# Performance work log

Hardware: AMD Instinct MI355X
Metric: run time of the kernel (lower is better)

The kernel has to match this reference:

```python
import jax, jax.numpy as jnp
import numpy as np

N_HEAD = 16
LORA_SCALE = 1.0 / 4.0  # alpha=1, r=4
LN_EPS = 1e-5


def _ln(x, g, b):
    # LayerNorm subclass casts to float32 then back to input dtype
    xf = x.astype(jnp.float32)
    m = xf.mean(-1, keepdims=True)
    v = xf.var(-1, keepdims=True)
    y = (xf - m) / jnp.sqrt(v + LN_EPS) * g + b
    return y.astype(x.dtype)


def _lora(h, a, b):
    # x @ a.T @ b.T * scaling ; a:[r,d], b:[d,r]
    return (h @ a.T) @ b.T * LORA_SCALE


def _attn(h, Wq, bq, Wk, Wv, bv, Wo, bo, la_k, lb_k, la_v, lb_v, la_o, lb_o):
    B, S, D = h.shape
    hd = D // N_HEAD
    scale = hd ** (-0.25)
    q = h @ Wq.T + bq
    k = h @ Wk.T + _lora(h, la_k, lb_k)          # key Linear has no bias
    v = h @ Wv.T + bv + _lora(h, la_v, lb_v)
    qh = q.reshape(B, S, N_HEAD, hd).transpose(0, 2, 1, 3) * scale  # [B,H,S,hd]
    kh = k.reshape(B, S, N_HEAD, hd).transpose(0, 2, 1, 3) * scale
    vh = v.reshape(B, S, N_HEAD, hd).transpose(0, 2, 1, 3)
    qk = jnp.einsum('bhqd,bhkd->bhqk', qh, kh).astype(jnp.float32)
    w = jax.nn.softmax(qk, axis=-1).astype(q.dtype)
    wv = jnp.einsum('bhqk,bhkd->bhqd', w, vh)
    wv = wv.transpose(0, 2, 1, 3).reshape(B, S, D)
    return wv @ Wo.T + bo + _lora(wv, la_o, lb_o)


def setup_inputs() -> dict:
    key = jax.random.key(0)
    D, R = 1024, 4
    B, S = 8, 1024
    ks = jax.random.split(key, 20)
    sd = 0.02
    inp = {
        'x': jax.random.normal(ks[0], (B, S, D), jnp.float32),
        'Wq': jax.random.normal(ks[1], (D, D), jnp.float32) * sd,
        'bq': jnp.zeros((D,), jnp.float32),
        'Wk': jax.random.normal(ks[2], (D, D), jnp.float32) * sd,
        'Wv': jax.random.normal(ks[3], (D, D), jnp.float32) * sd,
        'bv': jnp.zeros((D,), jnp.float32),
        'Wo': jax.random.normal(ks[4], (D, D), jnp.float32) * sd,
        'bo': jnp.zeros((D,), jnp.float32),
        'la_k': jax.random.normal(ks[5], (R, D), jnp.float32) * sd,
        'lb_k': jax.random.normal(ks[6], (D, R), jnp.float32) * sd,
        'la_v': jax.random.normal(ks[7], (R, D), jnp.float32) * sd,
        'lb_v': jax.random.normal(ks[8], (D, R), jnp.float32) * sd,
        'la_o': jax.random.normal(ks[9], (R, D), jnp.float32) * sd,
        'lb_o': jax.random.normal(ks[10], (D, R), jnp.float32) * sd,
        'g_attn': jnp.ones((D,), jnp.float32),
        'b_attn': jnp.zeros((D,), jnp.float32),
        'W1': jax.random.normal(ks[11], (4 * D, D), jnp.float32) * sd,
        'b1': jnp.zeros((4 * D,), jnp.float32),
        'W2': jax.random.normal(ks[12], (D, 4 * D), jnp.float32) * sd,
        'b2': jnp.zeros((D,), jnp.float32),
        'g_mlp': jnp.ones((D,), jnp.float32),
        'b_mlp': jnp.zeros((D,), jnp.float32),
    }
    return inp


def reference(x, Wq, bq, Wk, Wv, bv, Wo, bo, la_k, lb_k, la_v, lb_v, la_o, lb_o,
              g_attn, b_attn, W1, b1, W2, b2, g_mlp, b_mlp):
    # self-attention + residual (LoRA on key/value/out)
    x = x + _attn(_ln(x, g_attn, b_attn), Wq, bq, Wk, Wv, bv, Wo, bo,
                  la_k, lb_k, la_v, lb_v, la_o, lb_o)
    # MLP + residual (exact GELU, matching nn.GELU default)
    h = _ln(x, g_mlp, b_mlp)
    h = jax.nn.gelu(h @ W1.T + b1, approximate=False)
    x = x + h @ W2.T + b2
    return x
```

## Files before the change

kernel.cpp:

```cpp
#include <hip/hip_runtime.h>
#include <math.h>

typedef _Float16 f16_t;
typedef f16_t f16x8 __attribute__((ext_vector_type(8)));
typedef f16_t f16x4 __attribute__((ext_vector_type(4)));
typedef float f32x4 __attribute__((ext_vector_type(4)));
typedef float fv4 __attribute__((ext_vector_type(4)));

#define MFMA16(a, b, c) __builtin_amdgcn_mfma_f32_16x16x32_f16(a, b, c, 0, 0, 0)

__device__ __forceinline__ void gload16(const void* g, void* l) {
  __builtin_amdgcn_global_load_lds((const __attribute__((address_space(1))) void*)g,
                                   (__attribute__((address_space(3))) void*)l, 16, 0, 0);
}

__global__ __launch_bounds__(256) void ln_f32(const float* __restrict__ x,
                                              const float* __restrict__ g,
                                              const float* __restrict__ b,
                                              f16_t* __restrict__ y) {
  const int D = 1024;
  int row = blockIdx.x;
  int t = threadIdx.x;
  const float* xr = x + (size_t)row * D + t * 4;
  float x0 = xr[0], x1 = xr[1], x2 = xr[2], x3 = xr[3];
  float sum = x0 + x1 + x2 + x3;
  float sq = x0 * x0 + x1 * x1 + x2 * x2 + x3 * x3;
  for (int d = 32; d; d >>= 1) {
    sum += __shfl_down(sum, d);
    sq += __shfl_down(sq, d);
  }
  __shared__ float ssum[4], ssq[4];
  int w = t >> 6, lane = t & 63;
  if (lane == 0) { ssum[w] = sum; ssq[w] = sq; }
  __syncthreads();
  float ts = ssum[0] + ssum[1] + ssum[2] + ssum[3];
  float tq = ssq[0] + ssq[1] + ssq[2] + ssq[3];
  float mean = ts * (1.0f / 1024.0f);
  float var = tq * (1.0f / 1024.0f) - mean * mean;
  float rstd = rsqrtf(var + 1e-5f);
  f16_t* yr = y + (size_t)row * D + t * 4;
  const float* gr = g + t * 4;
  const float* br = b + t * 4;
  yr[0] = (f16_t)((x0 - mean) * rstd * gr[0] + br[0]);
  yr[1] = (f16_t)((x1 - mean) * rstd * gr[1] + br[1]);
  yr[2] = (f16_t)((x2 - mean) * rstd * gr[2] + br[2]);
  yr[3] = (f16_t)((x3 - mean) * rstd * gr[3] + br[3]);
}

__global__ __launch_bounds__(256) void ln_f16(const f16_t* __restrict__ x,
                                              const float* __restrict__ g,
                                              const float* __restrict__ b,
                                              f16_t* __restrict__ y) {
  const int D = 1024;
  int row = blockIdx.x;
  int t = threadIdx.x;
  const f16_t* xr = x + (size_t)row * D + t * 4;
  float x0 = (float)xr[0], x1 = (float)xr[1], x2 = (float)xr[2], x3 = (float)xr[3];
  float sum = x0 + x1 + x2 + x3;
  float sq = x0 * x0 + x1 * x1 + x2 * x2 + x3 * x3;
  for (int d = 32; d; d >>= 1) {
    sum += __shfl_down(sum, d);
    sq += __shfl_down(sq, d);
  }
  __shared__ float ssum[4], ssq[4];
  int w = t >> 6, lane = t & 63;
  if (lane == 0) { ssum[w] = sum; ssq[w] = sq; }
  __syncthreads();
  float ts = ssum[0] + ssum[1] + ssum[2] + ssum[3];
  float tq = ssq[0] + ssq[1] + ssq[2] + ssq[3];
  float mean = ts * (1.0f / 1024.0f);
  float var = tq * (1.0f / 1024.0f) - mean * mean;
  float rstd = rsqrtf(var + 1e-5f);
  f16_t* yr = y + (size_t)row * D + t * 4;
  const float* gr = g + t * 4;
  const float* br = b + t * 4;
  yr[0] = (f16_t)((x0 - mean) * rstd * gr[0] + br[0]);
  yr[1] = (f16_t)((x1 - mean) * rstd * gr[1] + br[1]);
  yr[2] = (f16_t)((x2 - mean) * rstd * gr[2] + br[2]);
  yr[3] = (f16_t)((x3 - mean) * rstd * gr[3] + br[3]);
}

__global__ __launch_bounds__(256) void convert_w(
    const float* __restrict__ wq, const float* __restrict__ wk,
    const float* __restrict__ wv, const float* __restrict__ wo,
    const float* __restrict__ w1, const float* __restrict__ w2,
    f16_t* __restrict__ oq, f16_t* __restrict__ ok, f16_t* __restrict__ ov,
    f16_t* __restrict__ oo, f16_t* __restrict__ o1, f16_t* __restrict__ o2) {
  int bid = blockIdx.x;
  const float* src;
  f16_t* dst;
  int bi;
  if (bid < 2048) {
    int seg = bid >> 9;
    bi = bid & 511;
    src = seg == 0 ? wq : seg == 1 ? wk : seg == 2 ? wv : wo;
    dst = seg == 0 ? oq : seg == 1 ? ok : seg == 2 ? ov : oo;
  } else if (bid < 4096) {
    bi = bid - 2048; src = w1; dst = o1;
  } else {
    bi = bid - 4096; src = w2; dst = o2;
  }
  size_t idx = (size_t)bi * 2048 + (size_t)threadIdx.x * 8;
  fv4 a = *(const fv4*)(src + idx);
  fv4 b = *(const fv4*)(src + idx + 4);
  f16x8 h;
#pragma unroll
  for (int j = 0; j < 4; ++j) { h[j] = (f16_t)a[j]; h[4 + j] = (f16_t)b[j]; }
  *(f16x8*)(dst + idx) = h;
}

__global__ __launch_bounds__(256) void lora_kv_kernel(
    const f16_t* __restrict__ h, const float* __restrict__ la_k,
    const float* __restrict__ la_v, float* __restrict__ t_k,
    float* __restrict__ t_v, int K) {
  int lane = threadIdx.x & 63;
  int w = threadIdx.x >> 6;
  int row = blockIdx.x * 4 + w;
  const f16_t* hrow = h + (size_t)row * K;
  float ak[4] = {0.f, 0.f, 0.f, 0.f};
  float av[4] = {0.f, 0.f, 0.f, 0.f};
  for (int it = 0; it < K / 512; ++it) {
    int base = it * 512 + lane * 8;
    f16x8 hx = *(const f16x8*)(hrow + base);
#pragma unroll
    for (int r = 0; r < 4; ++r) {
      const float* kr = la_k + (size_t)r * K + base;
      const float* vr = la_v + (size_t)r * K + base;
#pragma unroll
      for (int j = 0; j < 8; ++j) {
        float hv = (float)hx[j];
        ak[r] += hv * kr[j];
        av[r] += hv * vr[j];
      }
    }
  }
#pragma unroll
  for (int r = 0; r < 4; ++r) {
    for (int d = 32; d; d >>= 1) {
      ak[r] += __shfl_down(ak[r], d);
      av[r] += __shfl_down(av[r], d);
    }
  }
  if (lane == 0) {
#pragma unroll
    for (int r = 0; r < 4; ++r) {
      t_k[(size_t)row * 4 + r] = ak[r];
      t_v[(size_t)row * 4 + r] = av[r];
    }
  }
}

__global__ __launch_bounds__(256) void lora_t_kernel(const f16_t* __restrict__ h,
                                                     const float* __restrict__ la,
                                                     float* __restrict__ t, int K) {
  int lane = threadIdx.x & 63;
  int w = threadIdx.x >> 6;
  int row = blockIdx.x * 4 + w;
  const f16_t* hrow = h + (size_t)row * K;
  float acc[4] = {0.f, 0.f, 0.f, 0.f};
  for (int it = 0; it < K / 512; ++it) {
    int base = it * 512 + lane * 8;
    f16x8 hx = *(const f16x8*)(hrow + base);
#pragma unroll
    for (int r = 0; r < 4; ++r) {
      const float* ar = la + (size_t)r * K + base;
#pragma unroll
      for (int j = 0; j < 8; ++j) acc[r] += (float)hx[j] * ar[j];
    }
  }
#pragma unroll
  for (int r = 0; r < 4; ++r) {
    for (int d = 32; d; d >>= 1) acc[r] += __shfl_down(acc[r], d);
  }
  if (lane == 0) {
#pragma unroll
    for (int r = 0; r < 4; ++r) t[(size_t)row * 4 + r] = acc[r];
  }
}

__global__ __launch_bounds__(512, 2) void gemm_wide(
    const f16_t* __restrict__ A, const f16_t* __restrict__ B,
    const float* __restrict__ bias, const float* __restrict__ loraT,
    const float* __restrict__ loraB, const float* residf,
    const f16_t* __restrict__ residb, f16_t* Cb, float* Cf,
    int M, int N, int K, int ldb, int dogelu) {
  __shared__ __align__(16) f16_t Asm[8192];
  __shared__ __align__(16) f16_t Bsm[16384];
  const int tid = threadIdx.x;
  const int lane = tid & 63, wid = tid >> 6;
  const int wm = wid >> 2, wn = wid & 3;
  const int l15 = lane & 15, lhi = lane >> 4;
  int nwg = gridDim.x * gridDim.y;
  int bid = blockIdx.y * gridDim.x + blockIdx.x;
  int swz = (bid & 7) * (nwg >> 3) + (bid >> 3);
  const int m0 = (swz / gridDim.x) * 128, n0 = (swz % gridDim.x) * 256;
  const int arow = tid >> 3;
  const int aslot = tid & 7;

  f32x4 acc[4][4];
#pragma unroll
  for (int i = 0; i < 4; ++i)
#pragma unroll
    for (int j = 0; j < 4; ++j) acc[i][j] = (f32x4){0.f, 0.f, 0.f, 0.f};

  auto stageA = [&](int step) {
#pragma unroll
    for (int c = 0; c < 2; ++c) {
      int r = c * 64 + arow;
      int cm = aslot ^ (r & 7);
      gload16(A + (size_t)(m0 + r) * K + (size_t)step * 64 + cm * 8,
              (char*)Asm + c * 8192 + wid * 1024);
    }
  };
  auto stageB = [&](int step) {
#pragma unroll
    for (int c = 0; c < 4; ++c) {
      int r = c * 64 + arow;
      int cm = aslot ^ (r & 7);
      gload16(B + (size_t)(n0 + r) * ldb + (size_t)step * 64 + cm * 8,
              (char*)Bsm + c * 8192 + wid * 1024);
    }
  };

  const int nsteps = K >> 6;
  for (int t = 0; t < nsteps; ++t) {
    if (t) __syncthreads();
    stageA(t);
    stageB(t);
    __syncthreads();
#pragma unroll
    for (int kk = 0; kk < 2; ++kk) {
      f16x8 af[4], bf[4];
#pragma unroll
      for (int i = 0; i < 4; ++i) {
        int row = wm * 64 + i * 16 + l15;
        af[i] = *(const f16x8*)((char*)Asm + row * 128 +
                                ((kk * 64 + lhi * 16) ^ ((row & 7) << 4)));
      }
#pragma unroll
      for (int j = 0; j < 4; ++j) {
        int row = wn * 64 + j * 16 + l15;
        bf[j] = *(const f16x8*)((char*)Bsm + row * 128 +
                                ((kk * 64 + lhi * 16) ^ ((row & 7) << 4)));
      }
#pragma unroll
      for (int i = 0; i < 4; ++i)
#pragma unroll
        for (int j = 0; j < 4; ++j) acc[i][j] = MFMA16(af[i], bf[j], acc[i][j]);
    }
  }

  const int gm = m0 + wm * 64, gn = n0 + wn * 64;
#pragma unroll
  for (int j = 0; j < 4; ++j) {
    int gcol = gn + j * 16 + l15;
    float bj = bias ? bias[gcol] : 0.f;
    float lb0 = 0.f, lb1 = 0.f, lb2 = 0.f, lb3 = 0.f;
    if (loraB) {
      const float* p = loraB + (size_t)gcol * 4;
      lb0 = p[0]; lb1 = p[1]; lb2 = p[2]; lb3 = p[3];
    }
#pragma unroll
    for (int i = 0; i < 4; ++i) {
      float v4[4];
#pragma unroll
      for (int r = 0; r < 4; ++r) {
        int grow = gm + i * 16 + lhi * 4 + r;
        float val = acc[i][j][r] + bj;
        if (loraT) {
          const float* tp = loraT + (size_t)grow * 4;
          val += 0.25f * (tp[0] * lb0 + tp[1] * lb1 + tp[2] * lb2 + tp[3] * lb3);
        }
        if (dogelu) val = 0.5f * val * (1.0f + erff(val * 0.70710678118654752f));
        if (residf) val += residf[(size_t)grow * N + gcol];
        if (residb) val += (float)residb[(size_t)grow * N + gcol];
        v4[r] = val;
      }
      if (Cf) {
#pragma unroll
        for (int r = 0; r < 4; ++r)
          Cf[(size_t)(gm + i * 16 + lhi * 4 + r) * N + gcol] = v4[r];
      } else {
#pragma unroll
        for (int r = 0; r < 4; ++r)
          Cb[(size_t)(gm + i * 16 + lhi * 4 + r) * N + gcol] = (f16_t)v4[r];
      }
    }
  }
}

__global__ __launch_bounds__(512, 2) void gemm_qkv_wide(
    const f16_t* __restrict__ A, const f16_t* __restrict__ W,
    const float* __restrict__ bq, const float* __restrict__ bv,
    const float* __restrict__ t_k, const float* __restrict__ lb_k,
    const float* __restrict__ t_v, const float* __restrict__ lb_v,
    f16_t* __restrict__ Pq, f16_t* __restrict__ Pk, f16_t* __restrict__ Pvt,
    int K) {
  const int D = 1024;
  __shared__ __align__(16) f16_t Asm[8192];
  __shared__ __align__(16) f16_t Bsm[16384];
  const int tid = threadIdx.x;
  const int lane = tid & 63, wid = tid >> 6;
  const int wm = wid >> 2, wn = wid & 3;
  const int l15 = lane & 15, lhi = lane >> 4;
  int nwg = gridDim.x * gridDim.y;
  int bid = blockIdx.y * gridDim.x + blockIdx.x;
  int swz = (bid & 7) * (nwg >> 3) + (bid >> 3);
  const int m0 = (swz / gridDim.x) * 128, n0 = (swz % gridDim.x) * 256;
  const int seg = n0 >> 10;
  const int arow = tid >> 3;
  const int aslot = tid & 7;

  f32x4 acc[4][4];
#pragma unroll
  for (int i = 0; i < 4; ++i)
#pragma unroll
    for (int j = 0; j < 4; ++j) acc[i][j] = (f32x4){0.f, 0.f, 0.f, 0.f};

  auto stageA = [&](int step) {
#pragma unroll
    for (int c = 0; c < 2; ++c) {
      int r = c * 64 + arow;
      int cm = aslot ^ (r & 7);
      gload16(A + (size_t)(m0 + r) * K + (size_t)step * 64 + cm * 8,
              (char*)Asm + c * 8192 + wid * 1024);
    }
  };
  auto stageB = [&](int step) {
#pragma unroll
    for (int c = 0; c < 4; ++c) {
      int r = c * 64 + arow;
      int cm = aslot ^ (r & 7);
      gload16(W + (size_t)(n0 + r) * K + (size_t)step * 64 + cm * 8,
              (char*)Bsm + c * 8192 + wid * 1024);
    }
  };

  const int nsteps = K >> 6;
  for (int t = 0; t < nsteps; ++t) {
    if (t) __syncthreads();
    stageA(t);
    stageB(t);
    __syncthreads();
#pragma unroll
    for (int kk = 0; kk < 2; ++kk) {
      f16x8 af[4], bf[4];
#pragma unroll
      for (int i = 0; i < 4; ++i) {
        int row = wm * 64 + i * 16 + l15;
        af[i] = *(const f16x8*)((char*)Asm + row * 128 +
                                ((kk * 64 + lhi * 16) ^ ((row & 7) << 4)));
      }
#pragma unroll
      for (int j = 0; j < 4; ++j) {
        int row = wn * 64 + j * 16 + l15;
        bf[j] = *(const f16x8*)((char*)Bsm + row * 128 +
                                ((kk * 64 + lhi * 16) ^ ((row & 7) << 4)));
      }
#pragma unroll
      for (int i = 0; i < 4; ++i)
#pragma unroll
        for (int j = 0; j < 4; ++j) acc[i][j] = MFMA16(af[i], bf[j], acc[i][j]);
    }
  }

  const int gm = m0 + wm * 64, gn = n0 + wn * 64;
  const float* tB = (seg == 1) ? t_k : t_v;
#pragma unroll
  for (int j = 0; j < 4; ++j) {
    int gcol = gn + j * 16 + l15;
    int c = gcol & 1023;
    float bj = (seg == 0) ? bq[c] : (seg == 2 ? bv[c] : 0.f);
    float lb0 = 0.f, lb1 = 0.f, lb2 = 0.f, lb3 = 0.f;
    if (seg) {
      const float* p = (seg == 1 ? lb_k : lb_v) + (size_t)c * 4;
      lb0 = p[0]; lb1 = p[1]; lb2 = p[2]; lb3 = p[3];
    }
#pragma unroll
    for (int i = 0; i < 4; ++i) {
      float v4[4];
#pragma unroll
      for (int r = 0; r < 4; ++r) {
        int grow = gm + i * 16 + lhi * 4 + r;
        float val = acc[i][j][r] + bj;
        if (seg) {
          const float* tp = tB + (size_t)grow * 4;
          val += 0.25f * (tp[0] * lb0 + tp[1] * lb1 + tp[2] * lb2 + tp[3] * lb3);
        }
        v4[r] = val;
      }
      if (seg < 2) {
        f16_t* dst = (seg == 0) ? Pq : Pk;
#pragma unroll
        for (int r = 0; r < 4; ++r)
          dst[(size_t)(gm + i * 16 + lhi * 4 + r) * D + c] = (f16_t)v4[r];
      } else {
        int grow0 = gm + i * 16 + lhi * 4;
        int bb = grow0 >> 10, ss = grow0 & 1023;
        int hh = c >> 6, dd = c & 63;
        f16x4 pk;
#pragma unroll
        for (int r = 0; r < 4; ++r) pk[r] = (f16_t)v4[r];
        *(f16x4*)(Pvt + (((size_t)bb * 16 + hh) * 64 + dd) * 1024 + ss) = pk;
      }
    }
  }
}

__global__ __launch_bounds__(256, 2) void gemm_mfma(
    const f16_t* __restrict__ A, const float* __restrict__ B,
    const float* __restrict__ bias, const float* __restrict__ loraT,
    const float* __restrict__ loraB, const float* residf,
    const f16_t* __restrict__ residb, f16_t* Cb, float* Cf, f16_t* Cvt,
    int M, int N, int K, int ldb, int dogelu) {
  __shared__ __align__(16) f16_t smem[2][16384];
  const int tid = threadIdx.x;
  const int lane = tid & 63, wid = tid >> 6;
  const int wm = wid >> 1, wn = wid & 1;
  const int l15 = lane & 15, lhi = lane >> 4;
  const int m0 = blockIdx.y * 128, n0 = blockIdx.x * 128;
  const int arow = tid >> 3;
  const int aslot = tid & 7;

  f32x4 acc[4][4];
#pragma unroll
  for (int i = 0; i < 4; ++i)
#pragma unroll
    for (int j = 0; j < 4; ++j) acc[i][j] = (f32x4){0.f, 0.f, 0.f, 0.f};

  fv4 breg[4][2];

  auto stageA = [&](int step, int buf) {
#pragma unroll
    for (int c = 0; c < 4; ++c) {
      int r = c * 32 + arow;
      int cm = aslot ^ (r & 7);
      gload16(A + (size_t)(m0 + r) * K + (size_t)step * 64 + cm * 8,
              (char*)&smem[buf][0] + c * 4096 + wid * 1024);
    }
  };
  auto loadB = [&](int step) {
#pragma unroll
    for (int c = 0; c < 4; ++c) {
      int r = c * 32 + arow;
      const float* gp = B + (size_t)(n0 + r) * ldb + (size_t)step * 64 + aslot * 8;
      breg[c][0] = *(const fv4*)gp;
      breg[c][1] = *(const fv4*)(gp + 4);
    }
  };
  auto writeB = [&](int buf) {
#pragma unroll
    for (int c = 0; c < 4; ++c) {
      int r = c * 32 + arow;
      f16x8 hh;
#pragma unroll
      for (int j = 0; j < 4; ++j) hh[j] = (f16_t)breg[c][0][j];
#pragma unroll
      for (int j = 0; j < 4; ++j) hh[4 + j] = (f16_t)breg[c][1][j];
      int boff = r * 128 + ((aslot * 16) ^ ((r & 7) << 4));
      *(f16x8*)((char*)&smem[buf][8192] + boff) = hh;
    }
  };

  const int nsteps = K >> 6;
  stageA(0, 0);
  loadB(0);
  writeB(0);
  __syncthreads();
  for (int t = 0; t < nsteps; ++t) {
    int cur = t & 1, nxt = cur ^ 1;
    if (t + 1 < nsteps) { stageA(t + 1, nxt); loadB(t + 1); }
    const char* As = (const char*)&smem[cur][0];
    const char* Bs = (const char*)&smem[cur][8192];
#pragma unroll
    for (int kk = 0; kk < 2; ++kk) {
      f16x8 af[4], bf[4];
#pragma unroll
      for (int i = 0; i < 4; ++i) {
        int row = wm * 64 + i * 16 + l15;
        af[i] = *(const f16x8*)(As + row * 128 + ((kk * 64 + lhi * 16) ^ ((row & 7) << 4)));
      }
#pragma unroll
      for (int j = 0; j < 4; ++j) {
        int row = wn * 64 + j * 16 + l15;
        bf[j] = *(const f16x8*)(Bs + row * 128 + ((kk * 64 + lhi * 16) ^ ((row & 7) << 4)));
      }
#pragma unroll
      for (int i = 0; i < 4; ++i)
#pragma unroll
        for (int j = 0; j < 4; ++j) acc[i][j] = MFMA16(af[i], bf[j], acc[i][j]);
    }
    if (t + 1 < nsteps) writeB(nxt);
    __syncthreads();
  }

  const int gm = m0 + wm * 64, gn = n0 + wn * 64;
#pragma unroll
  for (int j = 0; j < 4; ++j) {
    int gcol = gn + j * 16 + l15;
    float bj = bias ? bias[gcol] : 0.f;
    float lb0 = 0.f, lb1 = 0.f, lb2 = 0.f, lb3 = 0.f;
    if (loraB) {
      const float* p = loraB + (size_t)gcol * 4;
      lb0 = p[0]; lb1 = p[1]; lb2 = p[2]; lb3 = p[3];
    }
#pragma unroll
    for (int i = 0; i < 4; ++i) {
      float v4[4];
#pragma unroll
      for (int r = 0; r < 4; ++r) {
        int grow = gm + i * 16 + lhi * 4 + r;
        float val = acc[i][j][r] + bj;
        if (loraT) {
          const float* tp = loraT + (size_t)grow * 4;
          val += 0.25f * (tp[0] * lb0 + tp[1] * lb1 + tp[2] * lb2 + tp[3] * lb3);
        }
        if (dogelu) val = 0.5f * val * (1.0f + erff(val * 0.70710678118654752f));
        if (residf) val += residf[(size_t)grow * N + gcol];
        if (residb) val += (float)residb[(size_t)grow * N + gcol];
        v4[r] = val;
      }
      if (Cf) {
#pragma unroll
        for (int r = 0; r < 4; ++r)
          Cf[(size_t)(gm + i * 16 + lhi * 4 + r) * N + gcol] = v4[r];
      } else if (Cvt) {
        int grow0 = gm + i * 16 + lhi * 4;
        int bb = grow0 >> 10, ss = grow0 & 1023;
        int hh = gcol >> 6, dd = gcol & 63;
        f16x4 pk;
#pragma unroll
        for (int r = 0; r < 4; ++r) pk[r] = (f16_t)v4[r];
        *(f16x4*)(Cvt + (((size_t)bb * 16 + hh) * 64 + dd) * 1024 + ss) = pk;
      } else {
#pragma unroll
        for (int r = 0; r < 4; ++r)
          Cb[(size_t)(gm + i * 16 + lhi * 4 + r) * N + gcol] = (f16_t)v4[r];
      }
    }
  }
}

__global__ __launch_bounds__(256, 3) void attn_mfma(const f16_t* __restrict__ q,
                                                    const f16_t* __restrict__ k,
                                                    const f16_t* __restrict__ vt,
                                                    f16_t* __restrict__ wv) {
  const int S = 1024, D = 1024;
  __shared__ __align__(16) f16_t Qs[128 * 64];
  __shared__ __align__(16) f16_t SP[128 * 64];
  __shared__ __align__(16) f16_t Ks[64 * 64];
  __shared__ __align__(16) f16_t Vts[64 * 64];
  __shared__ float rsb[128];
  __shared__ float lib[128];
  const int tid = threadIdx.x, lane = tid & 63, w = tid >> 6;
  const int l15 = lane & 15, lhi = lane >> 4;
  const int q0 = blockIdx.x * 128;
  const int h = blockIdx.y, b = blockIdx.z;
  const f16_t* qg = q + ((size_t)b * S + q0) * D + h * 64;
  const f16_t* kg = k + (size_t)b * S * D + h * 64;
  const f16_t* vg = vt + ((size_t)b * 16 + h) * 64 * (size_t)S;

#pragma unroll
  for (int c = 0; c < 4; ++c) {
    int r = c * 32 + (tid >> 3), kc = tid & 7;
    f16x8 xx = *(const f16x8*)(qg + (size_t)r * D + kc * 8);
    *(f16x8*)((char*)Qs + r * 128 + ((kc * 16) ^ ((r & 7) << 4))) = xx;
  }
  __syncthreads();
  f16x8 qf[2][2];
#pragma unroll
  for (int i = 0; i < 2; ++i) {
    int row = w * 32 + i * 16 + l15;
#pragma unroll
    for (int kk = 0; kk < 2; ++kk)
      qf[i][kk] = *(const f16x8*)((char*)Qs + row * 128 +
                                  ((kk * 64 + lhi * 16) ^ ((row & 7) << 4)));
  }

  f32x4 oacc[2][4];
#pragma unroll
  for (int i = 0; i < 2; ++i)
#pragma unroll
    for (int j = 0; j < 4; ++j) oacc[i][j] = (f32x4){0.f, 0.f, 0.f, 0.f};
  float m_run = -1e30f, l_run = 0.f;
  const int myrow = w * 32 + (lane >> 1);
  const int half = lane & 1;

  for (int kv = 0; kv < 16; ++kv) {
    __syncthreads();
#pragma unroll
    for (int c = 0; c < 2; ++c) {
      int r = c * 32 + (tid >> 3), kc = tid & 7;
      f16x8 xk = *(const f16x8*)(kg + (size_t)(kv * 64 + r) * D + kc * 8);
      *(f16x8*)((char*)Ks + r * 128 + ((kc * 16) ^ ((r & 7) << 4))) = xk;
      f16x8 xv = *(const f16x8*)(vg + (size_t)r * S + kv * 64 + kc * 8);
      *(f16x8*)((char*)Vts + r * 128 + ((kc * 16) ^ ((r & 7) << 4))) = xv;
    }
    __syncthreads();
    f32x4 sacc[2][4];
#pragma unroll
    for (int i = 0; i < 2; ++i)
#pragma unroll
      for (int j = 0; j < 4; ++j) sacc[i][j] = (f32x4){0.f, 0.f, 0.f, 0.f};
#pragma unroll
    for (int kk = 0; kk < 2; ++kk) {
      f16x8 kf[4];
#pragma unroll
      for (int j = 0; j < 4; ++j) {
        int row = j * 16 + l15;
        kf[j] = *(const f16x8*)((char*)Ks + row * 128 +
                                ((kk * 64 + lhi * 16) ^ ((row & 7) << 4)));
      }
#pragma unroll
      for (int i = 0; i < 2; ++i)
#pragma unroll
        for (int j = 0; j < 4; ++j) sacc[i][j] = MFMA16(qf[i][kk], kf[j], sacc[i][j]);
    }
#pragma unroll
    for (int i = 0; i < 2; ++i)
#pragma unroll
      for (int j = 0; j < 4; ++j)
#pragma unroll
        for (int r = 0; r < 4; ++r) {
          int srow = w * 32 + i * 16 + lhi * 4 + r;
          int scol = j * 16 + l15;
          *(f16_t*)((char*)SP + srow * 128 + ((scol * 2) ^ ((srow & 7) << 4))) =
              (f16_t)(sacc[i][j][r] * 0.125f);
        }
    __syncthreads();
    f16x8 ch[4];
#pragma unroll
    for (int c = 0; c < 4; ++c)
      ch[c] = *(const f16x8*)((char*)SP + myrow * 128 +
                              ((half * 64 + c * 16) ^ ((myrow & 7) << 4)));
    float mt = -1e30f;
#pragma unroll
    for (int c = 0; c < 4; ++c)
#pragma unroll
      for (int e = 0; e < 8; ++e) mt = fmaxf(mt, (float)ch[c][e]);
    mt = fmaxf(mt, __shfl_xor(mt, 1));
    float mnew = fmaxf(m_run, mt);
    float resc = __expf(m_run - mnew);
    float lsum = 0.f;
#pragma unroll
    for (int c = 0; c < 4; ++c) {
      f16x8 p8;
#pragma unroll
      for (int e = 0; e < 8; ++e) {
        float p = __expf((float)ch[c][e] - mnew);
        lsum += p;
        p8[e] = (f16_t)p;
      }
      *(f16x8*)((char*)SP + myrow * 128 + ((half * 64 + c * 16) ^ ((myrow & 7) << 4))) = p8;
    }
    lsum += __shfl_xor(lsum, 1);
    l_run = l_run * resc + lsum;
    m_run = mnew;
    if (half == 0) rsb[myrow] = resc;
    __syncthreads();
#pragma unroll
    for (int i = 0; i < 2; ++i) {
      float f0 = rsb[w * 32 + i * 16 + lhi * 4 + 0];
      float f1 = rsb[w * 32 + i * 16 + lhi * 4 + 1];
      float f2 = rsb[w * 32 + i * 16 + lhi * 4 + 2];
      float f3 = rsb[w * 32 + i * 16 + lhi * 4 + 3];
#pragma unroll
      for (int j = 0; j < 4; ++j) {
        oacc[i][j][0] *= f0;
        oacc[i][j][1] *= f1;
        oacc[i][j][2] *= f2;
        oacc[i][j][3] *= f3;
      }
    }
#pragma unroll
    for (int kk = 0; kk < 2; ++kk) {
      f16x8 pa[2], vb[4];
#pragma unroll
      for (int i = 0; i < 2; ++i) {
        int row = w * 32 + i * 16 + l15;
        pa[i] = *(const f16x8*)((char*)SP + row * 128 +
                                ((kk * 64 + lhi * 16) ^ ((row & 7) << 4)));
      }
#pragma unroll
      for (int j = 0; j < 4; ++j) {
        int row = j * 16 + l15;
        vb[j] = *(const f16x8*)((char*)Vts + row * 128 +
                                ((kk * 64 + lhi * 16) ^ ((row & 7) << 4)));
      }
#pragma unroll
      for (int i = 0; i < 2; ++i)
#pragma unroll
        for (int j = 0; j < 4; ++j) oacc[i][j] = MFMA16(pa[i], vb[j], oacc[i][j]);
    }
  }
  if (half == 0) lib[myrow] = 1.f / l_run;
  __syncthreads();
#pragma unroll
  for (int i = 0; i < 2; ++i)
#pragma unroll
    for (int r = 0; r < 4; ++r) {
      int row = w * 32 + i * 16 + lhi * 4 + r;
      float li = lib[row];
      size_t base = ((size_t)b * S + q0 + row) * D + h * 64;
#pragma unroll
      for (int j = 0; j < 4; ++j)
        wv[base + j * 16 + l15] = (f16_t)(oacc[i][j][r] * li);
    }
}

extern "C" void kernel_launch(void* const* d_in, const int* in_sizes, int n_in,
                              void* d_out, int out_size, void* d_ws, size_t ws_size,
                              hipStream_t stream) {
  const int B = 8, S = 1024, D = 1024, F = 4096;
  const int M = B * S;

  const float* x = (const float*)d_in[0];
  const float* Wq = (const float*)d_in[1];
  const float* bq = (const float*)d_in[2];
  const float* Wk = (const float*)d_in[3];
  const float* Wv = (const float*)d_in[4];
  const float* bv = (const float*)d_in[5];
  const float* Wo = (const float*)d_in[6];
  const float* bo = (const float*)d_in[7];
  const float* la_k = (const float*)d_in[8];
  const float* lb_k = (const float*)d_in[9];
  const float* la_v = (const float*)d_in[10];
  const float* lb_v = (const float*)d_in[11];
  const float* la_o = (const float*)d_in[12];
  const float* lb_o = (const float*)d_in[13];
  const float* g_attn = (const float*)d_in[14];
  const float* b_attn = (const float*)d_in[15];
  const float* W1 = (const float*)d_in[16];
  const float* b1 = (const float*)d_in[17];
  const float* W2 = (const float*)d_in[18];
  const float* b2 = (const float*)d_in[19];
  const float* g_mlp = (const float*)d_in[20];
  const float* b_mlp = (const float*)d_in[21];

  float* t_k = (float*)((char*)d_ws + 16);
  float* t_v = t_k + (size_t)M * 4;
  float* t_o = t_v + (size_t)M * 4;
  const size_t MD = (size_t)M * D;
  f16_t* P0 = (f16_t*)((char*)d_ws + 409600);
  f16_t* P1 = P0 + MD;
  f16_t* P2 = P0 + 2 * MD;
  f16_t* P3 = P0 + 3 * MD;
  f16_t* Wqkvf = P0 + 4 * MD;
  f16_t* Wof = Wqkvf + 3 * (size_t)D * D;
  f16_t* W1f = Wof + (size_t)D * D;
  f16_t* W2f = W1f + (size_t)F * D;
  float* outf = (float*)d_out;
  const size_t need = 409600 + 4 * MD * sizeof(f16_t) +
                      (4 * (size_t)D * D + 2 * (size_t)F * D) * sizeof(f16_t);
  const bool f16w = ws_size >= need;

  if (f16w)
    convert_w<<<6144, 256, 0, stream>>>(
        Wq, Wk, Wv, Wo, W1, W2, Wqkvf, Wqkvf + (size_t)D * D,
        Wqkvf + 2 * (size_t)D * D, Wof, W1f, W2f);

  ln_f32<<<M, 256, 0, stream>>>(x, g_attn, b_attn, P0);
  lora_kv_kernel<<<M / 4, 256, 0, stream>>>(P0, la_k, la_v, t_k, t_v, D);
  if (f16w) {
    gemm_qkv_wide<<<dim3(12, 64), 512, 0, stream>>>(
        P0, Wqkvf, bq, bv, t_k, lb_k, t_v, lb_v, P1, P2, P3, D);
  } else {
    gemm_mfma<<<dim3(8, 64), 256, 0, stream>>>(
        P0, Wq, bq, nullptr, nullptr, nullptr, nullptr, P1, nullptr, nullptr,
        M, D, D, D, 0);
    gemm_mfma<<<dim3(8, 64), 256, 0, stream>>>(
        P0, Wk, nullptr, t_k, lb_k, nullptr, nullptr, P2, nullptr, nullptr,
        M, D, D, D, 0);
    gemm_mfma<<<dim3(8, 64), 256, 0, stream>>>(
        P0, Wv, bv, t_v, lb_v, nullptr, nullptr, nullptr, nullptr, P3,
        M, D, D, D, 0);
  }
  attn_mfma<<<dim3(8, 16, 8), 256, 0, stream>>>(P1, P2, P3, P0);
  lora_t_kernel<<<M / 4, 256, 0, stream>>>(P0, la_o, t_o, D);
  if (f16w)
    gemm_wide<<<dim3(4, 64), 512, 0, stream>>>(
        P0, Wof, bo, t_o, lb_o, x, nullptr, P3, nullptr, M, D, D, D, 0);
  else
    gemm_mfma<<<dim3(8, 64), 256, 0, stream>>>(
        P0, Wo, bo, t_o, lb_o, x, nullptr, P3, nullptr, nullptr, M, D, D, D, 0);
  ln_f16<<<M, 256, 0, stream>>>(P3, g_mlp, b_mlp, P0);
  if (f16w) {
    gemm_wide<<<dim3(8, 64), 512, 0, stream>>>(
        P0, W1f, b1, nullptr, nullptr, nullptr, nullptr, P1, nullptr,
        M, 2048, D, D, 1);
    gemm_wide<<<dim3(4, 64), 512, 0, stream>>>(
        P1, W2f, b2, nullptr, nullptr, nullptr, P3, nullptr, outf,
        M, D, 2048, F, 0);
    gemm_wide<<<dim3(8, 64), 512, 0, stream>>>(
        P0, W1f + (size_t)2048 * D, b1 + 2048, nullptr, nullptr, nullptr, nullptr,
        P1, nullptr, M, 2048, D, D, 1);
    gemm_wide<<<dim3(4, 64), 512, 0, stream>>>(
        P1, W2f + 2048, nullptr, nullptr, nullptr, outf, nullptr, nullptr, outf,
        M, D, 2048, F, 0);
  } else {
    gemm_mfma<<<dim3(16, 64), 256, 0, stream>>>(
        P0, W1, b1, nullptr, nullptr, nullptr, nullptr, P1, nullptr, nullptr,
        M, 2048, D, D, 1);
    gemm_mfma<<<dim3(8, 64), 256, 0, stream>>>(
        P1, W2, b2, nullptr, nullptr, nullptr, P3, nullptr, outf, nullptr,
        M, D, 2048, F, 0);
    gemm_mfma<<<dim3(16, 64), 256, 0, stream>>>(
        P0, W1 + (size_t)2048 * D, b1 + 2048, nullptr, nullptr, nullptr, nullptr,
        P1, nullptr, nullptr, M, 2048, D, D, 1);
    gemm_mfma<<<dim3(8, 64), 256, 0, stream>>>(
        P1, W2 + 2048, nullptr, nullptr, nullptr, outf, nullptr, nullptr, outf,
        nullptr, M, D, 2048, F, 0);
  }
}
```

Baseline: 706.1 us.

## Triple-buffer GEMM LDS tiles with async prefetch and explicit vmcnt waits

Replaces the load-then-compute GEMM main loop with a three-stage LDS ring that prefetches tiles up to three steps ahead. It uses explicit s_waitcnt vmcnt counts, raw barriers and MFMA priority boosting. The aim is to hide global-to-LDS latency behind MFMA work, which the previous single-buffered loop fully exposed. The cost is LDS use rising to about 144KB per block, which likely allows only one 512-thread block per CU despite the launch bound of two.

```diff
diff --git a/kernel.cpp b/kernel.cpp
--- a/kernel.cpp
+++ b/kernel.cpp
@@ -178,14 +178,60 @@
   }
 }
 
-__global__ __launch_bounds__(512, 2) void gemm_wide(
+#define GEMM_PIPE_BODY                                                        \
+  f32x4 acc[4][4];                                                            \
+  _Pragma("unroll") for (int i = 0; i < 4; ++i)                               \
+      _Pragma("unroll") for (int j = 0; j < 4; ++j)                           \
+          acc[i][j] = (f32x4){0.f, 0.f, 0.f, 0.f};                            \
+  const int nsteps = K >> 6;                                                  \
+  stageA(0, 0); stageB(0, 0);                                                 \
+  stageA(1, 1); stageB(1, 1);                                                 \
+  stageA(2, 2); stageB(2, 2);                                                 \
+  int b3 = 0;                                                                 \
+  for (int kt = 0; kt < nsteps; ++kt) {                                       \
+    if (kt + 2 < nsteps)                                                      \
+      asm volatile("s_waitcnt vmcnt(12)" ::: "memory");                       \
+    else if (kt + 1 < nsteps)                                                 \
+      asm volatile("s_waitcnt vmcnt(6)" ::: "memory");                        \
+    else                                                                      \
+      asm volatile("s_waitcnt vmcnt(0)" ::: "memory");                        \
+    __builtin_amdgcn_sched_barrier(0);                                        \
+    __builtin_amdgcn_s_barrier();                                             \
+    f16x8 af[4][2], bf[4][2];                                                 \
+    _Pragma("unroll") for (int kk = 0; kk < 2; ++kk) {                        \
+      _Pragma("unroll") for (int i = 0; i < 4; ++i) {                         \
+        int row = wm * 64 + i * 16 + l15;                                     \
+        af[i][kk] = *(const f16x8*)((const char*)Abuf[b3] + row * 128 +       \
+                                    ((kk * 64 + lhi * 16) ^ ((row & 7) << 4)));\
+      }                                                                       \
+      _Pragma("unroll") for (int j = 0; j < 4; ++j) {                         \
+        int row = wn * 64 + j * 16 + l15;                                     \
+        bf[j][kk] = *(const f16x8*)((const char*)Bbuf[b3] + row * 128 +       \
+                                    ((kk * 64 + lhi * 16) ^ ((row & 7) << 4)));\
+      }                                                                       \
+    }                                                                         \
+    asm volatile("s_waitcnt lgkmcnt(0)" ::: "memory");                        \
+    __builtin_amdgcn_sched_barrier(0);                                        \
+    __builtin_amdgcn_s_barrier();                                             \
+    if (kt + 3 < nsteps) { stageA(kt + 3, b3); stageB(kt + 3, b3); }          \
+    __builtin_amdgcn_sched_barrier(0);                                        \
+    __builtin_amdgcn_s_setprio(1);                                            \
+    _Pragma("unroll") for (int kk = 0; kk < 2; ++kk)                          \
+        _Pragma("unroll") for (int i = 0; i < 4; ++i)                         \
+            _Pragma("unroll") for (int j = 0; j < 4; ++j)                     \
+                acc[i][j] = MFMA16(af[i][kk], bf[j][kk], acc[i][j]);          \
+    __builtin_amdgcn_s_setprio(0);                                            \
+    b3 = (b3 == 2) ? 0 : b3 + 1;                                              \
+  }
+
+__global__ __launch_bounds__(512, 2) void gemm_pipe(
     const f16_t* __restrict__ A, const f16_t* __restrict__ B,
     const float* __restrict__ bias, const float* __restrict__ loraT,
     const float* __restrict__ loraB, const float* residf,
     const f16_t* __restrict__ residb, f16_t* Cb, float* Cf,
     int M, int N, int K, int ldb, int dogelu) {
-  __shared__ __align__(16) f16_t Asm[8192];
-  __shared__ __align__(16) f16_t Bsm[16384];
+  __shared__ __align__(16) f16_t Abuf[3][8192];
+  __shared__ __align__(16) f16_t Bbuf[3][16384];
   const int tid = threadIdx.x;
   const int lane = tid & 63, wid = tid >> 6;
   const int wm = wid >> 2, wn = wid & 3;
@@ -197,58 +243,26 @@
   const int arow = tid >> 3;
   const int aslot = tid & 7;
 
-  f32x4 acc[4][4];
-#pragma unroll
-  for (int i = 0; i < 4; ++i)
-#pragma unroll
-    for (int j = 0; j < 4; ++j) acc[i][j] = (f32x4){0.f, 0.f, 0.f, 0.f};
-
-  auto stageA = [&](int step) {
+  auto stageA = [&](int step, int buf) {
 #pragma unroll
     for (int c = 0; c < 2; ++c) {
       int r = c * 64 + arow;
       int cm = aslot ^ (r & 7);
       gload16(A + (size_t)(m0 + r) * K + (size_t)step * 64 + cm * 8,
-              (char*)Asm + c * 8192 + wid * 1024);
+              (char*)Abuf[buf] + c * 8192 + wid * 1024);
     }
   };
-  auto stageB = [&](int step) {
+  auto stageB = [&](int step, int buf) {
 #pragma unroll
     for (int c = 0; c < 4; ++c) {
       int r = c * 64 + arow;
       int cm = aslot ^ (r & 7);
       gload16(B + (size_t)(n0 + r) * ldb + (size_t)step * 64 + cm * 8,
-              (char*)Bsm + c * 8192 + wid * 1024);
+              (char*)Bbuf[buf] + c * 8192 + wid * 1024);
     }
   };
 
-  const int nsteps = K >> 6;
-  for (int t = 0; t < nsteps; ++t) {
-    if (t) __syncthreads();
-    stageA(t);
-    stageB(t);
-    __syncthreads();
-#pragma unroll
-    for (int kk = 0; kk < 2; ++kk) {
-      f16x8 af[4], bf[4];
-#pragma unroll
-      for (int i = 0; i < 4; ++i) {
-        int row = wm * 64 + i * 16 + l15;
-        af[i] = *(const f16x8*)((char*)Asm + row * 128 +
-                                ((kk * 64 + lhi * 16) ^ ((row & 7) << 4)));
-      }
-#pragma unroll
-      for (int j = 0; j < 4; ++j) {
-        int row = wn * 64 + j * 16 + l15;
-        bf[j] = *(const f16x8*)((char*)Bsm + row * 128 +
-                                ((kk * 64 + lhi * 16) ^ ((row & 7) << 4)));
-      }
-#pragma unroll
-      for (int i = 0; i < 4; ++i)
-#pragma unroll
-        for (int j = 0; j < 4; ++j) acc[i][j] = MFMA16(af[i], bf[j], acc[i][j]);
-    }
-  }
+  GEMM_PIPE_BODY
 
   const int gm = m0 + wm * 64, gn = n0 + wn * 64;
 #pragma unroll
@@ -289,7 +303,7 @@
   }
 }
 
-__global__ __launch_bounds__(512, 2) void gemm_qkv_wide(
+__global__ __launch_bounds__(512, 2) void gemm_qkv_pipe(
     const f16_t* __restrict__ A, const f16_t* __restrict__ W,
     const float* __restrict__ bq, const float* __restrict__ bv,
     const float* __restrict__ t_k, const float* __restrict__ lb_k,
@@ -297,8 +311,8 @@
     f16_t* __restrict__ Pq, f16_t* __restrict__ Pk, f16_t* __restrict__ Pvt,
     int K) {
   const int D = 1024;
-  __shared__ __align__(16) f16_t Asm[8192];
-  __shared__ __align__(16) f16_t Bsm[16384];
+  __shared__ __align__(16) f16_t Abuf[3][8192];
+  __shared__ __align__(16) f16_t Bbuf[3][16384];
   const int tid = threadIdx.x;
   const int lane = tid & 63, wid = tid >> 6;
   const int wm = wid >> 2, wn = wid & 3;
@@ -311,58 +325,26 @@
   const int arow = tid >> 3;
   const int aslot = tid & 7;
 
-  f32x4 acc[4][4];
-#pragma unroll
-  for (int i = 0; i < 4; ++i)
-#pragma unroll
-    for (int j = 0; j < 4; ++j) acc[i][j] = (f32x4){0.f, 0.f, 0.f, 0.f};
-
-  auto stageA = [&](int step) {
+  auto stageA = [&](int step, int buf) {
 #pragma unroll
     for (int c = 0; c < 2; ++c) {
       int r = c * 64 + arow;
       int cm = aslot ^ (r & 7);
       gload16(A + (size_t)(m0 + r) * K + (size_t)step * 64 + cm * 8,
-              (char*)Asm + c * 8192 + wid * 1024);
+              (char*)Abuf[buf] + c * 8192 + wid * 1024);
     }
   };
-  auto stageB = [&](int step) {
+  auto stageB = [&](int step, int buf) {
 #pragma unroll
     for (int c = 0; c < 4; ++c) {
       int r = c * 64 + arow;
       int cm = aslot ^ (r & 7);
       gload16(W + (size_t)(n0 + r) * K + (size_t)step * 64 + cm * 8,
-              (char*)Bsm + c * 8192 + wid * 1024);
+              (char*)Bbuf[buf] + c * 8192 + wid * 1024);
     }
   };
 
-  const int nsteps = K >> 6;
-  for (int t = 0; t < nsteps; ++t) {
-    if (t) __syncthreads();
-    stageA(t);
-    stageB(t);
-    __syncthreads();
-#pragma unroll
-    for (int kk = 0; kk < 2; ++kk) {
-      f16x8 af[4], bf[4];
-#pragma unroll
-      for (int i = 0; i < 4; ++i) {
-        int row = wm * 64 + i * 16 + l15;
-        af[i] = *(const f16x8*)((char*)Asm + row * 128 +
-                                ((kk * 64 + lhi * 16) ^ ((row & 7) << 4)));
-      }
-#pragma unroll
-      for (int j = 0; j < 4; ++j) {
-        int row = wn * 64 + j * 16 + l15;
-        bf[j] = *(const f16x8*)((char*)Bsm + row * 128 +
-                                ((kk * 64 + lhi * 16) ^ ((row & 7) << 4)));
-      }
-#pragma unroll
-      for (int i = 0; i < 4; ++i)
-#pragma unroll
-        for (int j = 0; j < 4; ++j) acc[i][j] = MFMA16(af[i], bf[j], acc[i][j]);
-    }
-  }
+  GEMM_PIPE_BODY
 
   const int gm = m0 + wm * 64, gn = n0 + wn * 64;
   const float* tB = (seg == 1) ? t_k : t_v;
@@ -762,7 +744,7 @@
   ln_f32<<<M, 256, 0, stream>>>(x, g_attn, b_attn, P0);
   lora_kv_kernel<<<M / 4, 256, 0, stream>>>(P0, la_k, la_v, t_k, t_v, D);
   if (f16w) {
-    gemm_qkv_wide<<<dim3(12, 64), 512, 0, stream>>>(
+    gemm_qkv_pipe<<<dim3(12, 64), 512, 0, stream>>>(
         P0, Wqkvf, bq, bv, t_k, lb_k, t_v, lb_v, P1, P2, P3, D);
   } else {
     gemm_mfma<<<dim3(8, 64), 256, 0, stream>>>(
@@ -778,23 +760,23 @@
   attn_mfma<<<dim3(8, 16, 8), 256, 0, stream>>>(P1, P2, P3, P0);
   lora_t_kernel<<<M / 4, 256, 0, stream>>>(P0, la_o, t_o, D);
   if (f16w)
-    gemm_wide<<<dim3(4, 64), 512, 0, stream>>>(
+    gemm_pipe<<<dim3(4, 64), 512, 0, stream>>>(
         P0, Wof, bo, t_o, lb_o, x, nullptr, P3, nullptr, M, D, D, D, 0);
   else
     gemm_mfma<<<dim3(8, 64), 256, 0, stream>>>(
         P0, Wo, bo, t_o, lb_o, x, nullptr, P3, nullptr, nullptr, M, D, D, D, 0);
   ln_f16<<<M, 256, 0, stream>>>(P3, g_mlp, b_mlp, P0);
   if (f16w) {
-    gemm_wide<<<dim3(8, 64), 512, 0, stream>>>(
+    gemm_pipe<<<dim3(8, 64), 512, 0, stream>>>(
         P0, W1f, b1, nullptr, nullptr, nullptr, nullptr, P1, nullptr,
         M, 2048, D, D, 1);
-    gemm_wide<<<dim3(4, 64), 512, 0, stream>>>(
+    gemm_pipe<<<dim3(4, 64), 512, 0, stream>>>(
         P1, W2f, b2, nullptr, nullptr, nullptr, P3, nullptr, outf,
         M, D, 2048, F, 0);
-    gemm_wide<<<dim3(8, 64), 512, 0, stream>>>(
+    gemm_pipe<<<dim3(8, 64), 512, 0, stream>>>(
         P0, W1f + (size_t)2048 * D, b1 + 2048, nullptr, nullptr, nullptr, nullptr,
         P1, nullptr, M, 2048, D, D, 1);
-    gemm_wide<<<dim3(4, 64), 512, 0, stream>>>(
+    gemm_pipe<<<dim3(4, 64), 512, 0, stream>>>(
         P1, W2f + 2048, nullptr, nullptr, nullptr, outf, nullptr, nullptr, outf,
         M, D, 2048, F, 0);
   } else {
```

New measurement: 646.7 us. 8.4% less time.
